# Optimization experiments

Hardware: AMD Instinct MI355X
Metric: run time of the kernel (lower is better)

Reference implementation:

```python
import jax, jax.numpy as jnp
import numpy as np

B, C, H, W = 4, 256, 64, 64
Q = 150          # num_queries
HID = 1024       # q_after hidden size
NEG = 1e9


def setup_inputs() -> dict:
    key = jax.random.key(0)
    ks = jax.random.split(key, 12)
    img_feat = jax.random.normal(ks[0], (B, C, H, W), jnp.float32)
    exe_feat = jax.random.normal(ks[1], (B, C, 7, 7), jnp.float32)
    mask = jax.random.randint(ks[2], (B, H, W), 0, 2).astype(jnp.float32)
    # parameters (similarity init = identity + small noise for a non-degenerate test)
    S = jnp.eye(C, dtype=jnp.float32) + 0.02 * jax.random.normal(ks[3], (C, C), jnp.float32)
    Wv = jax.random.normal(ks[4], (C, C), jnp.float32) / np.sqrt(C)
    ln_g = jnp.ones((C + 1,), jnp.float32)
    ln_b = jnp.zeros((C + 1,), jnp.float32)
    W1 = jax.random.normal(ks[5], (HID, C + 1), jnp.float32) / np.sqrt(C + 1)
    b1 = jnp.zeros((HID,), jnp.float32)
    W2 = jax.random.normal(ks[6], (C + 1, HID), jnp.float32) / np.sqrt(HID)
    b2 = jnp.zeros((C + 1,), jnp.float32)
    return {"img_feat": img_feat, "exe_feat": exe_feat, "mask": mask, "S": S,
            "Wv": Wv, "ln_g": ln_g, "ln_b": ln_b, "W1": W1, "b1": b1, "W2": W2, "b2": b2}


def _get_queries(simil):
    # simil: [B,H,W] detached heatmap; local-maxima NMS then top-k
    c1 = simil[:, :-1] >= simil[:, 1:]
    c2 = simil[:, 1:] > simil[:, :-1]
    c3 = simil[:, :, :-1] >= simil[:, :, 1:]
    c4 = simil[:, :, 1:] > simil[:, :, :-1]
    interior = c1[:, 1:, 1:-1] & c2[:, :-1, 1:-1] & c3[:, 1:-1, 1:] & c4[:, 1:-1, :-1]
    is_max = jnp.zeros(simil.shape, bool).at[:, 1:-1, 1:-1].set(interior)
    sup = jnp.where(is_max, simil, simil - NEG)
    _, q_ids = jax.lax.top_k(sup.reshape(simil.shape[0], -1), Q)   # [B,Q]
    coords = jnp.stack([q_ids // W, q_ids % W], axis=2)            # [B,Q,2]
    return q_ids, coords


def _forward(img_feat, exe_feat, mask, S, Wv, ln_g, ln_b, W1, b1, W2, b2):
    b, c, h, w = img_feat.shape
    hw = h * w
    unrolled = img_feat.reshape(b, c, hw)                               # [B,C,HW]
    exe = exe_feat.mean(axis=(2, 3))[:, :, None]                        # [B,C,1]
    concat = jnp.concatenate([unrolled, exe], axis=2)                   # [B,C,HW+1]
    values = jnp.einsum('bcn,dc->bnd', concat, Wv)                      # [B,HW+1,C]
    attn = jnp.einsum('bcm,cd,bdn->bmn', unrolled, S, concat)           # [B,HW,HW+1]
    hm = attn[:, :, -1].reshape(b, 1, h, w)
    q_ids, coords = _get_queries(jax.lax.stop_gradient(attn[:, :, -1]).reshape(b, h, w))
    # mask bias: outer product of pixel mask, exemplar column always allowed
    m2 = mask.reshape(b, hw, 1) * mask.reshape(b, 1, hw)
    m2 = jnp.concatenate([m2, jnp.ones((b, hw, 1), m2.dtype)], axis=2)
    attn = attn - (m2 != 1).astype(attn.dtype) * NEG
    attn = jax.nn.softmax(attn, axis=2)
    new_img = jnp.einsum('bmn,bnd->bmd', attn, values)                  # [B,HW,C]
    img_out = new_img.transpose(0, 2, 1).reshape(b, c, h, w) + img_feat
    img_out = jnp.concatenate([img_out, hm], axis=1)                    # [B,C+1,H,W]
    # gather query vectors at NMS peak locations
    q = jnp.take_along_axis(img_out.reshape(b, c + 1, hw), q_ids[:, None, :], axis=2)
    q = q.transpose(0, 2, 1)                                            # [B,Q,C+1]
    # q_after: LayerNorm -> Linear(1024) -> ReLU -> Linear(C+1)
    mu = q.mean(-1, keepdims=True)
    var = ((q - mu) ** 2).mean(-1, keepdims=True)
    qn = (q - mu) / jnp.sqrt(var + 1e-5) * ln_g + ln_b
    q_out = jax.nn.relu(qn @ W1.T + b1) @ W2.T + b2
    return img_out, q_out, coords


def reference(img_feat, exe_feat, mask, S, Wv, ln_g, ln_b, W1, b1, W2, b2):
    return _forward(img_feat, exe_feat, mask, S, Wv, ln_g, ln_b, W1, b1, W2, b2)
```

## Files before the change

kernel.cpp:

```cpp
#include <hip/hip_runtime.h>
#include <hip/hip_bf16.h>
#include <stdint.h>

typedef unsigned short u16;
typedef unsigned int u32;
typedef unsigned long long u64;
typedef __attribute__((ext_vector_type(8))) unsigned short u16x8;
typedef __attribute__((ext_vector_type(8))) short short8;
typedef __attribute__((ext_vector_type(4))) float f32x4;

#define CB   4
#define CC   256
#define CHW  4096
#define CNQ  4097
#define NQP  150
#define CHID 1024
#define XTROWS 4160
#define VROW   4160

#define XT_OFF   0ul
#define VB_OFF   (XT_OFF  + (size_t)CB*XTROWS*CC*2)
#define ST_OFF   (VB_OFF  + (size_t)CB*CC*VROW*2)
#define EXE_OFF  (ST_OFF  + 131072ul)
#define ZL_OFF   (EXE_OFF + 4096ul)
#define HEAT_OFF (ZL_OFF  + 4096ul)
#define QID_OFF  (HEAT_OFF+ 65536ul)
#define W1T_OFF  (QID_OFF + 2560ul)
#define W2T_OFF  (W1T_OFF + 1052672ul)
#define HB_OFF   (W2T_OFF + 1052672ul)

__device__ __forceinline__ u16 f2b(float f){
  __hip_bfloat16 h = __float2bfloat16(f); u16 r; __builtin_memcpy(&r, &h, 2); return r;
}
__device__ __forceinline__ f32x4 mfma16(u16x8 a, u16x8 b, f32x4 c){
  short8 as, bs; __builtin_memcpy(&as, &a, 16); __builtin_memcpy(&bs, &b, 16);
  return __builtin_amdgcn_mfma_f32_16x16x32_bf16(as, bs, c, 0, 0, 0);
}
__device__ __forceinline__ u16x8 zero8(){
  u16x8 v;
  #pragma unroll
  for (int e = 0; e < 8; e++) v[e] = 0;
  return v;
}
__device__ __forceinline__ u16x8 cvt8(f32x4 a, f32x4 b){
  u16x8 v;
  v[0]=f2b(a[0]); v[1]=f2b(a[1]); v[2]=f2b(a[2]); v[3]=f2b(a[3]);
  v[4]=f2b(b[0]); v[5]=f2b(b[1]); v[6]=f2b(b[2]); v[7]=f2b(b[3]);
  return v;
}
__device__ __forceinline__ void glds16(const u16* gp, u16* lp){
  __builtin_amdgcn_global_load_lds(
      (const __attribute__((address_space(1))) u32*)gp,
      (__attribute__((address_space(3))) u32*)lp, 16, 0, 0);
}

#define DPPF(x, ctrl) __int_as_float(__builtin_amdgcn_mov_dpp(__float_as_int(x), (ctrl), 0xF, 0xF, true))
__device__ __forceinline__ float red16_max(float x){
  x = fmaxf(x, DPPF(x, 0xB1));
  x = fmaxf(x, DPPF(x, 0x4E));
  x = fmaxf(x, DPPF(x, 0x141));
  x = fmaxf(x, DPPF(x, 0x140));
  return x;
}
__device__ __forceinline__ float red16_sum(float x){
  x += DPPF(x, 0xB1);
  x += DPPF(x, 0x4E);
  x += DPPF(x, 0x141);
  x += DPPF(x, 0x140);
  return x;
}

__device__ __forceinline__ void tpose_body(const float* __restrict__ src,
    float* __restrict__ dst, int R, int C, int bx, int by, char* sbuf){
  float (*tile)[33] = (float(*)[33])sbuf;
  int c0 = bx*32, r0 = by*32;
  int tc = threadIdx.x & 31, tr = threadIdx.x >> 5;
  for (int i = tr; i < 32; i += 8){
    int r = r0 + i, c = c0 + tc;
    tile[i][tc] = (r < R && c < C) ? src[(long)r*C + c] : 0.f;
  }
  __syncthreads();
  for (int i = tr; i < 32; i += 8){
    int c = c0 + i, r = r0 + tc;
    if (c < C && r < R) dst[(long)c*R + r] = tile[tc][i];
  }
}

__device__ __forceinline__ void t64_body(const float* __restrict__ src,
    u16* __restrict__ dst, int srcLd, long srcBatch, int dstLd, long dstBatch,
    int swz, int bx, int by, int bz, char* sbuf, u16* __restrict__ vb){
  u16 (*tile)[72] = (u16(*)[72])sbuf;
  int c0 = bx*64, m0 = by*64;
  const float* S = src + (long)bz*srcBatch;
  u16* D = dst + (long)bz*dstBatch;
  int t = threadIdx.x;
  int r = t >> 2, q = t & 3;
  for (int uu = q; uu < 8; uu += 4){
    const float* p = S + (long)(c0+r)*srcLd + m0 + uu*8;
    f32x4 a0 = *(const f32x4*)p;
    f32x4 a1 = *(const f32x4*)(p + 4);
    *(u16x8*)&tile[r][uu*8] = cvt8(a0, a1);
  }
  __syncthreads();
  for (int uu = q; uu < 8; uu += 4){
    u16x8 v;
    #pragma unroll
    for (int e = 0; e < 8; e++) v[e] = tile[uu*8 + e][r];
    int gidx = (c0 >> 3) + uu;
    if (swz) gidx ^= (r & 7)*4;
    *(u16x8*)(D + (long)(m0+r)*dstLd + gidx*8) = v;
  }
  if (vb){
    int c = c0 + r, cx = c & 7;
    u16* drow = vb + ((long)bz*CC + c)*VROW + m0;
    #pragma unroll
    for (int uu = q; uu < 8; uu += 4){
      u16x8 v = *(const u16x8*)&tile[r][uu*8];
      *(u16x8*)(drow + (uu ^ cx)*8) = v;
    }
  }
}

__global__ __launch_bounds__(256) void prep_k(
    const float* __restrict__ exe, const float* __restrict__ S,
    const float* __restrict__ W1, const float* __restrict__ W2,
    float* __restrict__ zl, u16* __restrict__ Xt, u16* __restrict__ Vb,
    u16* __restrict__ St, float* __restrict__ W1t, float* __restrict__ W2t){
  __shared__ __align__(16) char sbuf[9216];
  int id = blockIdx.x, t = threadIdx.x;
  if (id < 4){
    float* em = (float*)sbuf;
    int b = id;
    const float* p = exe + (b*CC + t)*49;
    float s = 0.f;
    for (int i = 0; i < 49; i++) s += p[i];
    float m = s / 49.f;
    em[t] = m;
    u16* xb = Xt + (size_t)b*XTROWS*CC;
    xb[(size_t)CHW*CC + t] = f2b(m);
    for (int i = 0; i < 63; i++)
      xb[(size_t)(CHW + 1 + i)*CC + t] = 0;
    {
      int cx = t & 7;
      u16* drow = Vb + ((long)b*CC + t)*VROW;
      #pragma unroll
      for (int gl = 0; gl < 8; gl++)
        *(u16x8*)(drow + (512 + gl)*8) = zero8();
      drow[(512 + cx)*8] = f2b(m);
    }
    __syncthreads();
    const float* Sr = S + (long)t*CC;
    float z = 0.f;
    for (int d = 0; d < CC; d++) z += Sr[d] * em[d];
    zl[b*CC + t] = z;
  } else if (id < 292){
    int i = id - 4;
    tpose_body(W1, W1t, CHID, 257, i % 9, i / 9, sbuf);
  } else if (id < 580){
    int i = id - 292;
    tpose_body(W2, W2t, 257, CHID, i % 32, i / 32, sbuf);
  } else {
    int i = id - 580;
    t64_body(S, St, CC, 0, CC, 0, 0, i & 3, i >> 2, 0, sbuf, nullptr);
  }
}

__global__ __launch_bounds__(256) void big_k(
    const float* __restrict__ img, const float* __restrict__ zl,
    u16* __restrict__ Xt, u16* __restrict__ Vb,
    float* __restrict__ heat, float* __restrict__ out_img){
  __shared__ __align__(16) char sbuf[9216];
  int id = blockIdx.x, t = threadIdx.x;
  if (id < 1024){
    int bx = id & 3, by = (id >> 2) & 63, bz = id >> 8;
    t64_body(img, Xt, CHW, (long)CC*CHW, CC, (long)XTROWS*CC, 1, bx, by, bz,
             sbuf, Vb);
  } else {
    int i = id - 1024;
    int bx = i & 15, b = i >> 4;
    float* z = (float*)sbuf;
    z[t] = zl[b*CC + t];
    __syncthreads();
    int m = bx*256 + t;
    const float* base = img + (long)b*CC*CHW + m;
    float s = 0.f;
    for (int c = 0; c < CC; c++) s += base[(long)c*CHW] * z[c];
    heat[b*CHW + m] = s;
    out_img[(long)b*257*CHW + (long)256*CHW + m] = s;
  }
}

__global__ __launch_bounds__(1024) void topk_k(const float* __restrict__ heat,
                                               int* __restrict__ qids,
                                               float* __restrict__ out_coords){
  int b = blockIdx.x, t = threadIdx.x;
  __shared__ unsigned long long sk[4096];
  const float* hb = heat + (long)b*CHW;
  for (int p = t; p < 4096; p += 1024){
    int i = p >> 6, j = p & 63;
    float h = hb[p];
    bool ismax = false;
    if (i >= 1 && i < 63 && j >= 1 && j < 63){
      ismax = (h >= hb[p+64]) && (h > hb[p-64]) && (h >= hb[p+1]) && (h > hb[p-1]);
    }
    float sup = ismax ? h : (h - 1e9f);
    unsigned u = __float_as_uint(sup);
    u = (u & 0x80000000u) ? ~u : (u | 0x80000000u);
    unsigned long long key = ((unsigned long long)u << 32) | (unsigned)(0xFFFFFFFFu - (unsigned)p);
    sk[p] = ~key;
  }
  __syncthreads();
  for (int k = 2; k <= 4096; k <<= 1){
    for (int j = k >> 1; j > 0; j >>= 1){
      for (int tt = t; tt < 2048; tt += 1024){
        int i1 = 2*tt - (tt & (j-1));
        int i2 = i1 + j;
        unsigned long long a = sk[i1], c = sk[i2];
        bool up = ((i1 & k) == 0);
        if (up ? (a > c) : (a < c)){ sk[i1] = c; sk[i2] = a; }
      }
      __syncthreads();
    }
  }
  if (t < NQP){
    unsigned long long key = ~sk[t];
    int p = (int)(0xFFFFFFFFu - (unsigned)(key & 0xFFFFFFFFull));
    qids[b*160 + t] = p;
    out_coords[((long)b*NQP + t)*2 + 0] = (float)(p >> 6);
    out_coords[((long)b*NQP + t)*2 + 1] = (float)(p & 63);
  }
}

__global__ __launch_bounds__(512, 2) void flash_k(
    const u16* __restrict__ Xt, const u16* __restrict__ St,
    const u16* __restrict__ Vb, const float* __restrict__ imgf,
    const float* __restrict__ maskp, const float* __restrict__ Wv,
    float* __restrict__ out_img){
  __shared__ __align__(16) char smem[144384];
  u16*   kp0 = (u16*)smem;
  u16*   kt0 = (u16*)(smem + 32768);
  u16*   kp1 = (u16*)(smem + 65536);
  u16*   kt1 = (u16*)(smem + 98304);
  u16*   p_tile = (u16*)(smem + 131072);
  unsigned char* maskb = (unsigned char*)(smem + 139264);
  float* mlx = (float*)(smem + 143360);

  int f = blockIdx.x;
  int l = (f & 7)*32 + (f >> 3);
  int b = l >> 6;
  int m0 = (l & 63)*64;
  int t = threadIdx.x;
  int lane = t & 63, l15 = lane & 15, qd = lane >> 4;
  int w = t >> 6, wm = w & 3, wn = w >> 2;
  f32x4 zero4 = {0.f,0.f,0.f,0.f};

  {
    const float* mp = maskp + (long)b*CHW + t*8;
    f32x4 a0 = *(const f32x4*)mp;
    f32x4 a1 = *(const f32x4*)(mp + 4);
    unsigned long long pk = 0;
    #pragma unroll
    for (int e = 0; e < 4; e++){
      pk |= (unsigned long long)(a0[e] == 1.0f ? 1u : 0u) << (8*e);
      pk |= (unsigned long long)(a1[e] == 1.0f ? 1u : 0u) << (8*(e+4));
    }
    *(unsigned long long*)&maskb[t*8] = pk;
  }

  const u16* xtb = Xt + (size_t)b*XTROWS*CC;
  const u16* vbb = Vb + (size_t)b*CC*VROW;

  {
    f32x4 D[8];
    #pragma unroll
    for (int i = 0; i < 8; i++) D[i] = zero4;
    const u16* arow = xtb + (long)(m0 + wm*16 + l15)*CC;
    int rsw = (l15 & 7)*4;
    #pragma unroll
    for (int ks = 0; ks < 8; ks++){
      u16x8 af = *(const u16x8*)(arow + ((ks*4 + qd) ^ rsw)*8);
      #pragma unroll
      for (int ds = 0; ds < 8; ds++){
        int dsg = wn*8 + ds;
        u16x8 bf_ = *(const u16x8*)(St + (long)(dsg*16 + l15)*CC + ks*32 + qd*8);
        D[ds] = mfma16(af, bf_, D[ds]);
      }
    }
    #pragma unroll
    for (int ds = 0; ds < 8; ds++){
      #pragma unroll
      for (int r = 0; r < 4; r++){
        int prow = wm*16 + qd*4 + r;
        int ccol = (wn*8 + ds)*16 + l15;
        kp0[prow*256 + ((ccol >> 3) ^ ((prow & 7)*4))*8 + (ccol & 7)] = f2b(D[ds][r]);
      }
    }
  }
  __syncthreads();
  u16x8 afrag[8];
  {
    int arl = wm*16 + l15;
    #pragma unroll
    for (int ks = 0; ks < 8; ks++)
      afrag[ks] = *(const u16x8*)&kp0[arl*256 + (((ks*4 + qd)) ^ ((arl & 7)*4))*8];
  }
  int rowAllowed[4];
  float mi[4], li[4];
  #pragma unroll
  for (int r = 0; r < 4; r++){
    int m = m0 + wm*16 + qd*4 + r;
    rowAllowed[r] = maskb[m];
    mi[r] = -1e30f; li[r] = 0.f;
  }
  f32x4 O[16];
  #pragma unroll
  for (int i = 0; i < 16; i++) O[i] = zero4;
  __syncthreads();

  {
    const u16* ksrc = xtb + w*2048 + lane*8;
    u16* kl = kp0 + w*2048;
    glds16(ksrc,        kl);
    glds16(ksrc + 512,  kl + 512);
    glds16(ksrc + 1024, kl + 1024);
    glds16(ksrc + 1536, kl + 1536);
    const u16* vsrc = vbb + (long)(w*32 + (lane >> 3))*VROW + (lane & 7)*8;
    u16* vl = kt0 + w*2048;
    glds16(vsrc,            vl);
    glds16(vsrc + 8*VROW,   vl + 512);
    glds16(vsrc + 16*VROW,  vl + 1024);
    glds16(vsrc + 24*VROW,  vl + 1536);
  }
  __syncthreads();

  for (int nt = 0; nt < 65; nt++){
    int cur = nt & 1;
    const u16* kpc = cur ? kp1 : kp0;
    const u16* ktc = cur ? kt1 : kt0;
    u16* kpn = cur ? kp0 : kp1;
    u16* ktn = cur ? kt0 : kt1;
    int n0 = nt*64;

    if (nt < 64){
      int n1 = n0 + 64;
      const u16* ksrc = xtb + (long)n1*CC + w*2048 + lane*8;
      u16* kl = kpn + w*2048;
      glds16(ksrc,        kl);
      glds16(ksrc + 512,  kl + 512);
      glds16(ksrc + 1024, kl + 1024);
      glds16(ksrc + 1536, kl + 1536);
      const u16* vsrc = vbb + (long)(w*32 + (lane >> 3))*VROW + n1 + (lane & 7)*8;
      u16* vl = ktn + w*2048;
      glds16(vsrc,            vl);
      glds16(vsrc + 8*VROW,   vl + 512);
      glds16(vsrc + 16*VROW,  vl + 1024);
      glds16(vsrc + 24*VROW,  vl + 1536);
    }

    f32x4 sc[2];
    sc[0] = zero4; sc[1] = zero4;
    __builtin_amdgcn_s_setprio(1);
    #pragma unroll
    for (int ks = 0; ks < 8; ks++){
      #pragma unroll
      for (int ns = 0; ns < 2; ns++){
        int n_l = (wn*2 + ns)*16 + l15;
        u16x8 bfrag = *(const u16x8*)&kpc[n_l*256 + (((ks*4 + qd)) ^ ((n_l & 7)*4))*8];
        sc[ns] = mfma16(afrag[ks], bfrag, sc[ns]);
      }
    }
    __builtin_amdgcn_s_setprio(0);

    float sEff[2][4];
    #pragma unroll
    for (int ns = 0; ns < 2; ns++){
      int n = n0 + (wn*2 + ns)*16 + l15;
      bool inv = (n >= CNQ);
      bool isEx = (n == CHW);
      int cm = 0;
      if (!inv && !isEx) cm = maskb[n];
      #pragma unroll
      for (int r = 0; r < 4; r++){
        float s = sc[ns][r];
        float se;
        if (inv)        se = -1e30f;
        else if (isEx)  se = s;
        else            se = (rowAllowed[r] & cm) ? s : s - 1e9f;
        sEff[ns][r] = se;
      }
    }
    float al[4], nm[4];
    #pragma unroll
    for (int r = 0; r < 4; r++){
      float tm = red16_max(fmaxf(sEff[0][r], sEff[1][r]));
      float newm = fmaxf(mi[r], tm);
      al[r] = (mi[r] < -1e29f) ? 0.f : __expf(fmaxf(mi[r] - newm, -88.f));
      nm[r] = newm; mi[r] = newm;
    }
    #pragma unroll
    for (int r = 0; r < 4; r++){
      float rs = 0.f;
      int prow = wm*16 + qd*4 + r;
      #pragma unroll
      for (int ns = 0; ns < 2; ns++){
        float p = __expf(fmaxf(sEff[ns][r] - nm[r], -88.f));
        rs += p;
        int ccol = (wn*2 + ns)*16 + l15;
        p_tile[prow*64 + ((ccol >> 3) ^ (prow & 7))*8 + (ccol & 7)] = f2b(p);
      }
      li[r] = li[r]*al[r] + red16_sum(rs);
    }
    asm volatile("s_waitcnt lgkmcnt(0)" ::: "memory");

    int needre = (al[0] != 1.f) | (al[1] != 1.f) | (al[2] != 1.f) | (al[3] != 1.f);
    if (__any(needre)){
      #pragma unroll
      for (int ds = 0; ds < 16; ds++){
        #pragma unroll
        for (int r = 0; r < 4; r++) O[ds][r] *= al[r];
      }
    }
    {
      int prow2 = wm*16 + l15;
      u16x8 pf = *(const u16x8*)&p_tile[prow2*64 + (((wn*4 + qd)) ^ (prow2 & 7))*8];
      __builtin_amdgcn_s_setprio(1);
      #pragma unroll
      for (int ds = 0; ds < 16; ds++){
        int c = ds*16 + l15;
        u16x8 vf = *(const u16x8*)&ktc[c*64 + (((wn*4 + qd)) ^ (c & 7))*8];
        O[ds] = mfma16(pf, vf, O[ds]);
      }
      __builtin_amdgcn_s_setprio(0);
    }
    __syncthreads();
  }

  if (l15 == 0){
    #pragma unroll
    for (int r = 0; r < 4; r++){
      mlx[(((wm*2 + wn)*16) + qd*4 + r)*2 + 0] = mi[r];
      mlx[(((wm*2 + wn)*16) + qd*4 + r)*2 + 1] = li[r];
    }
  }
  __syncthreads();
  float alpha[4], linv[4];
  #pragma unroll
  for (int r = 0; r < 4; r++){
    float mo = mlx[(((wm*2 + (1 - wn))*16) + qd*4 + r)*2 + 0];
    float lo = mlx[(((wm*2 + (1 - wn))*16) + qd*4 + r)*2 + 1];
    float ms = fmaxf(mi[r], mo);
    float aS = (mi[r] < -1e29f) ? 0.f : __expf(mi[r] - ms);
    float aO = (mo    < -1e29f) ? 0.f : __expf(mo - ms);
    float ls = li[r]*aS + lo*aO;
    alpha[r] = aS;
    linv[r] = (ls > 0.f) ? (1.0f / ls) : 0.f;
  }
  float* Tsum = (float*)smem;
  if (wn == 1){
    #pragma unroll
    for (int ds = 0; ds < 16; ds++){
      #pragma unroll
      for (int r = 0; r < 4; r++)
        Tsum[(wm*16 + qd*4 + r)*256 + ds*16 + l15] = O[ds][r]*alpha[r];
    }
  }
  __syncthreads();
  if (wn == 0){
    #pragma unroll
    for (int ds = 0; ds < 16; ds++){
      #pragma unroll
      for (int r = 0; r < 4; r++)
        O[ds][r] = (O[ds][r]*alpha[r] + Tsum[(wm*16 + qd*4 + r)*256 + ds*16 + l15]) * linv[r];
    }
  }
  __syncthreads();
  if (wn == 0){
    #pragma unroll
    for (int ds = 0; ds < 16; ds++){
      #pragma unroll
      for (int r = 0; r < 4; r++){
        int prow = wm*16 + qd*4 + r;
        int ccol = ds*16 + l15;
        kp0[prow*256 + ((ccol >> 3) ^ ((prow & 7)*4))*8 + (ccol & 7)] = f2b(O[ds][r]);
      }
    }
  }
  __syncthreads();
  u16x8 tfrag[8];
  {
    int arl = wm*16 + l15;
    #pragma unroll
    for (int ks = 0; ks < 8; ks++)
      tfrag[ks] = *(const u16x8*)&kp0[arl*256 + (((ks*4 + qd)) ^ ((arl & 7)*4))*8];
  }
  f32x4 F[8];
  #pragma unroll
  for (int i = 0; i < 8; i++) F[i] = zero4;
  #pragma unroll
  for (int ks = 0; ks < 8; ks++){
    #pragma unroll
    for (int ds = 0; ds < 8; ds++){
      int dsg = wn*8 + ds;
      const float* wr = Wv + (long)(dsg*16 + l15)*CC + ks*32 + qd*8;
      f32x4 w0 = *(const f32x4*)wr;
      f32x4 w1 = *(const f32x4*)(wr + 4);
      F[ds] = mfma16(tfrag[ks], cvt8(w0, w1), F[ds]);
    }
  }

  float* oi = out_img + (long)b*257*CHW;
  const float* fi = imgf + (long)b*CC*CHW;
  int mb = m0 + wm*16 + qd*4;
  #pragma unroll
  for (int ds = 0; ds < 8; ds++){
    int d = (wn*8 + ds)*16 + l15;
    f32x4 ivals = *(const f32x4*)(fi + (long)d*CHW + mb);
    f32x4 ovals;
    #pragma unroll
    for (int r = 0; r < 4; r++) ovals[r] = F[ds][r] + ivals[r];
    *(f32x4*)(oi + (long)d*CHW + mb) = ovals;
  }
}

__global__ __launch_bounds__(256) void qhead1_k(const float* __restrict__ out_img,
    const int* __restrict__ qids,
    const float* __restrict__ g, const float* __restrict__ be,
    const float* __restrict__ W1t, const float* __restrict__ b1,
    float* __restrict__ Hb){
  int hc = blockIdx.x, rb = blockIdx.y;
  int t = threadIdx.x, lane = t & 63, wv = t >> 6;
  __shared__ __align__(16) float xl[4][260];
  {
    int gq = rb*4 + wv;
    int b = gq / NQP, q = gq - b*NQP;
    int m = qids[b*160 + q];
    const float* oib = out_img + (long)b*257*CHW + m;
    float v[4];
    #pragma unroll
    for (int j = 0; j < 4; j++) v[j] = oib[(long)(lane + j*64)*CHW];
    float v4 = (lane == 0) ? oib[(long)256*CHW] : 0.f;
    float s = v[0]+v[1]+v[2]+v[3]+v4;
    #pragma unroll
    for (int d = 1; d < 64; d <<= 1) s += __shfl_xor(s, d, 64);
    float mu = s / 257.f;
    float d4 = (lane == 0) ? (v4 - mu) : 0.f;
    float vs = d4*d4;
    #pragma unroll
    for (int j = 0; j < 4; j++){ float dd = v[j]-mu; vs += dd*dd; }
    #pragma unroll
    for (int d = 1; d < 64; d <<= 1) vs += __shfl_xor(vs, d, 64);
    float inv = 1.0f / sqrtf(vs/257.f + 1e-5f);
    #pragma unroll
    for (int j = 0; j < 4; j++)
      xl[wv][lane + j*64] = (v[j]-mu)*inv*g[lane + j*64] + be[lane + j*64];
    if (lane == 0) xl[wv][256] = d4*inv*g[256] + be[256];
  }
  __syncthreads();
  int h = hc*256 + t;
  float acc0=0.f, acc1=0.f, acc2=0.f, acc3=0.f;
  #pragma unroll 8
  for (int c = 0; c < 256; c++){
    float wv_ = W1t[(long)c*CHID + h];
    acc0 += wv_*xl[0][c]; acc1 += wv_*xl[1][c];
    acc2 += wv_*xl[2][c]; acc3 += wv_*xl[3][c];
  }
  {
    float wv_ = W1t[(long)256*CHID + h];
    acc0 += wv_*xl[0][256]; acc1 += wv_*xl[1][256];
    acc2 += wv_*xl[2][256]; acc3 += wv_*xl[3][256];
  }
  float bb = b1[h];
  float* hb = Hb + (long)rb*4*CHID + h;
  hb[0]       = fmaxf(acc0 + bb, 0.f);
  hb[CHID]    = fmaxf(acc1 + bb, 0.f);
  hb[2*CHID]  = fmaxf(acc2 + bb, 0.f);
  hb[3*CHID]  = fmaxf(acc3 + bb, 0.f);
}

__global__ __launch_bounds__(256) void qhead2_k(float* __restrict__ qbuf,
    const float* __restrict__ Hb, const float* __restrict__ W2t,
    const float* __restrict__ b2){
  int rb = blockIdx.x;
  int t = threadIdx.x, lane = t & 63, wv = t >> 6;
  __shared__ __align__(16) float hl[4][CHID];
  const float* hs = Hb + (long)rb*4*CHID;
  #pragma unroll
  for (int q = 0; q < 4; q++)
    *(f32x4*)&hl[q][t*4] = *(const f32x4*)&hs[(long)q*CHID + t*4];
  __syncthreads();
  float a0=0.f, a1=0.f, a2=0.f, a3=0.f;
  #pragma unroll 8
  for (int c = 0; c < CHID; c++){
    float wv_ = W2t[(long)c*257 + t];
    a0 += wv_*hl[0][c]; a1 += wv_*hl[1][c];
    a2 += wv_*hl[2][c]; a3 += wv_*hl[3][c];
  }
  float bb = b2[t];
  qbuf[(long)(rb*4 + 0)*257 + t] = a0 + bb;
  qbuf[(long)(rb*4 + 1)*257 + t] = a1 + bb;
  qbuf[(long)(rb*4 + 2)*257 + t] = a2 + bb;
  qbuf[(long)(rb*4 + 3)*257 + t] = a3 + bb;
  if (wv == 0){
    float p0=0.f, p1=0.f, p2=0.f, p3=0.f;
    #pragma unroll
    for (int k = 0; k < 16; k++){
      int c = lane*16 + k;
      float wv_ = W2t[(long)c*257 + 256];
      p0 += wv_*hl[0][c]; p1 += wv_*hl[1][c];
      p2 += wv_*hl[2][c]; p3 += wv_*hl[3][c];
    }
    #pragma unroll
    for (int d = 1; d < 64; d <<= 1){
      p0 += __shfl_xor(p0, d, 64); p1 += __shfl_xor(p1, d, 64);
      p2 += __shfl_xor(p2, d, 64); p3 += __shfl_xor(p3, d, 64);
    }
    if (lane == 0){
      float b256 = b2[256];
      qbuf[(long)(rb*4 + 0)*257 + 256] = p0 + b256;
      qbuf[(long)(rb*4 + 1)*257 + 256] = p1 + b256;
      qbuf[(long)(rb*4 + 2)*257 + 256] = p2 + b256;
      qbuf[(long)(rb*4 + 3)*257 + 256] = p3 + b256;
    }
  }
}

extern "C" void kernel_launch(void* const* d_in, const int* in_sizes, int n_in,
                              void* d_out, int out_size, void* d_ws, size_t ws_size,
                              hipStream_t stream){
  (void)out_size; (void)ws_size;
  int idxImg=-1, idxExe=-1, idxMask=-1, idxB1=-1;
  int idx65[2]={-1,-1}; int n65=0;
  int idx263[2]={-1,-1}; int n263=0;
  int idx257[3]={-1,-1,-1}; int n257=0;
  for (int i = 0; i < n_in; i++){
    int s = in_sizes[i];
    if      (s == 4194304) idxImg = i;
    else if (s == 50176)   idxExe = i;
    else if (s == 16384)   idxMask = i;
    else if (s == 1024)    idxB1 = i;
    else if (s == 65536)  { if (n65 < 2)  idx65[n65++] = i; }
    else if (s == 263168) { if (n263 < 2) idx263[n263++] = i; }
    else if (s == 257)    { if (n257 < 3) idx257[n257++] = i; }
  }
  const float* img  = (const float*)d_in[idxImg];
  const float* exe  = (const float*)d_in[idxExe];
  const float* mask = (const float*)d_in[idxMask];
  const float* S    = (const float*)d_in[idx65[0]];
  const float* Wv   = (const float*)d_in[idx65[1]];
  const float* W1   = (const float*)d_in[idx263[0]];
  const float* W2   = (const float*)d_in[idx263[1]];
  const float* b1   = (const float*)d_in[idxB1];
  const float *lng, *lnb, *b2;
  if (idxImg == 0){
    lng = (const float*)d_in[idx257[0]];
    lnb = (const float*)d_in[idx257[1]];
    b2  = (const float*)d_in[idx257[2]];
  } else {
    b2  = (const float*)d_in[idx257[0]];
    lnb = (const float*)d_in[idx257[1]];
    lng = (const float*)d_in[idx257[2]];
  }

  char* ws = (char*)d_ws;
  u16*   Xt   = (u16*)(ws + XT_OFF);
  u16*   Vb   = (u16*)(ws + VB_OFF);
  u16*   St   = (u16*)(ws + ST_OFF);
  float* zl   = (float*)(ws + ZL_OFF);
  float* heat = (float*)(ws + HEAT_OFF);
  int*   qids = (int*)(ws + QID_OFF);
  float* W1t  = (float*)(ws + W1T_OFF);
  float* W2t  = (float*)(ws + W2T_OFF);
  float* Hb   = (float*)(ws + HB_OFF);

  float* out      = (float*)d_out;
  float* out_img  = out;
  float* qbuf     = out + (size_t)CB*257*CHW;
  float* out_crd  = qbuf + (size_t)CB*NQP*257;

  prep_k<<<dim3(596), dim3(256), 0, stream>>>(
      exe, S, W1, W2, zl, Xt, Vb, St, W1t, W2t);
  big_k<<<dim3(1088), dim3(256), 0, stream>>>(
      img, zl, Xt, Vb, heat, out_img);
  topk_k<<<dim3(CB), dim3(1024), 0, stream>>>(heat, qids, out_crd);
  flash_k<<<dim3(256), dim3(512), 0, stream>>>(
      Xt, St, Vb, img, mask, Wv, out_img);
  qhead1_k<<<dim3(4, CB*NQP/4), dim3(256), 0, stream>>>(
      out_img, qids, lng, lnb, W1t, b1, Hb);
  qhead2_k<<<dim3(CB*NQP/4), dim3(256), 0, stream>>>(qbuf, Hb, W2t, b2);
}
```

Baseline: 400.8 us.

## Split flash attention over key halves with a separate merge kernel

```diff
diff --git a/kernel.cpp b/kernel.cpp
--- a/kernel.cpp
+++ b/kernel.cpp
@@ -28,6 +28,8 @@
 #define W1T_OFF  (QID_OFF + 2560ul)
 #define W2T_OFF  (W1T_OFF + 1052672ul)
 #define HB_OFF   (W2T_OFF + 1052672ul)
+#define OP_OFF   (HB_OFF  + 2457600ul)
+#define ML_OFF   (OP_OFF  + (size_t)512*64*256*4)
 
 __device__ __forceinline__ u16 f2b(float f){
   __hip_bfloat16 h = __float2bfloat16(f); u16 r; __builtin_memcpy(&r, &h, 2); return r;
@@ -233,22 +235,24 @@
 
 __global__ __launch_bounds__(512, 2) void flash_k(
     const u16* __restrict__ Xt, const u16* __restrict__ St,
-    const u16* __restrict__ Vb, const float* __restrict__ imgf,
-    const float* __restrict__ maskp, const float* __restrict__ Wv,
-    float* __restrict__ out_img){
-  __shared__ __align__(16) char smem[144384];
-  u16*   kp0 = (u16*)smem;
-  u16*   kt0 = (u16*)(smem + 32768);
-  u16*   kp1 = (u16*)(smem + 65536);
-  u16*   kt1 = (u16*)(smem + 98304);
-  u16*   p_tile = (u16*)(smem + 131072);
-  unsigned char* maskb = (unsigned char*)(smem + 139264);
-  float* mlx = (float*)(smem + 143360);
+    const u16* __restrict__ Vb, const float* __restrict__ maskp,
+    float* __restrict__ Opart, float* __restrict__ MLpart){
+  __shared__ __align__(16) char smem[78848];
+  u16*   kp = (u16*)smem;
+  u16*   kt = (u16*)(smem + 32768);
+  u16*   p_tile = (u16*)(smem + 65536);
+  unsigned char* maskb = (unsigned char*)(smem + 73728);
+  float* mlx = (float*)(smem + 77824);
 
   int f = blockIdx.x;
-  int l = (f & 7)*32 + (f >> 3);
-  int b = l >> 6;
-  int m0 = (l & 63)*64;
+  int b = (f & 7) >> 1;
+  int half = f & 1;
+  int mt = f >> 3;
+  int m0 = mt*64;
+  int ntBeg = half ? 33 : 0;
+  int ntEnd = half ? 65 : 33;
+  int pid = (b*64 + mt)*2 + half;
+
   int t = threadIdx.x;
   int lane = t & 63, l15 = lane & 15, qd = lane >> 4;
   int w = t >> 6, wm = w & 3, wn = w >> 2;
@@ -292,7 +296,7 @@
       for (int r = 0; r < 4; r++){
         int prow = wm*16 + qd*4 + r;
         int ccol = (wn*8 + ds)*16 + l15;
-        kp0[prow*256 + ((ccol >> 3) ^ ((prow & 7)*4))*8 + (ccol & 7)] = f2b(D[ds][r]);
+        kp[prow*256 + ((ccol >> 3) ^ ((prow & 7)*4))*8 + (ccol & 7)] = f2b(D[ds][r]);
       }
     }
   }
@@ -302,7 +306,7 @@
     int arl = wm*16 + l15;
     #pragma unroll
     for (int ks = 0; ks < 8; ks++)
-      afrag[ks] = *(const u16x8*)&kp0[arl*256 + (((ks*4 + qd)) ^ ((arl & 7)*4))*8];
+      afrag[ks] = *(const u16x8*)&kp[arl*256 + (((ks*4 + qd)) ^ ((arl & 7)*4))*8];
   }
   int rowAllowed[4];
   float mi[4], li[4];
@@ -317,45 +321,26 @@
   for (int i = 0; i < 16; i++) O[i] = zero4;
   __syncthreads();
 
-  {
-    const u16* ksrc = xtb + w*2048 + lane*8;
-    u16* kl = kp0 + w*2048;
-    glds16(ksrc,        kl);
-    glds16(ksrc + 512,  kl + 512);
-    glds16(ksrc + 1024, kl + 1024);
-    glds16(ksrc + 1536, kl + 1536);
-    const u16* vsrc = vbb + (long)(w*32 + (lane >> 3))*VROW + (lane & 7)*8;
-    u16* vl = kt0 + w*2048;
-    glds16(vsrc,            vl);
-    glds16(vsrc + 8*VROW,   vl + 512);
-    glds16(vsrc + 16*VROW,  vl + 1024);
-    glds16(vsrc + 24*VROW,  vl + 1536);
-  }
-  __syncthreads();
-
-  for (int nt = 0; nt < 65; nt++){
-    int cur = nt & 1;
-    const u16* kpc = cur ? kp1 : kp0;
-    const u16* ktc = cur ? kt1 : kt0;
-    u16* kpn = cur ? kp0 : kp1;
-    u16* ktn = cur ? kt0 : kt1;
+#define STAGE(n0_) do { \
+    const u16* ksrc_ = xtb + (long)(n0_)*CC + w*2048 + lane*8; \
+    u16* kl_ = kp + w*2048; \
+    glds16(ksrc_,        kl_); \
+    glds16(ksrc_ + 512,  kl_ + 512); \
+    glds16(ksrc_ + 1024, kl_ + 1024); \
+    glds16(ksrc_ + 1536, kl_ + 1536); \
+    const u16* vsrc_ = vbb + (long)(w*32 + (lane >> 3))*VROW + (n0_) + (lane & 7)*8; \
+    u16* vl_ = kt + w*2048; \
+    glds16(vsrc_,            vl_); \
+    glds16(vsrc_ + 8*VROW,   vl_ + 512); \
+    glds16(vsrc_ + 16*VROW,  vl_ + 1024); \
+    glds16(vsrc_ + 24*VROW,  vl_ + 1536); \
+  } while(0)
+
+  STAGE(ntBeg*64);
+  __syncthreads();
+
+  for (int nt = ntBeg; nt < ntEnd; nt++){
     int n0 = nt*64;
-
-    if (nt < 64){
-      int n1 = n0 + 64;
-      const u16* ksrc = xtb + (long)n1*CC + w*2048 + lane*8;
-      u16* kl = kpn + w*2048;
-      glds16(ksrc,        kl);
-      glds16(ksrc + 512,  kl + 512);
-      glds16(ksrc + 1024, kl + 1024);
-      glds16(ksrc + 1536, kl + 1536);
-      const u16* vsrc = vbb + (long)(w*32 + (lane >> 3))*VROW + n1 + (lane & 7)*8;
-      u16* vl = ktn + w*2048;
-      glds16(vsrc,            vl);
-      glds16(vsrc + 8*VROW,   vl + 512);
-      glds16(vsrc + 16*VROW,  vl + 1024);
-      glds16(vsrc + 24*VROW,  vl + 1536);
-    }
 
     f32x4 sc[2];
     sc[0] = zero4; sc[1] = zero4;
@@ -365,7 +350,7 @@
       #pragma unroll
       for (int ns = 0; ns < 2; ns++){
         int n_l = (wn*2 + ns)*16 + l15;
-        u16x8 bfrag = *(const u16x8*)&kpc[n_l*256 + (((ks*4 + qd)) ^ ((n_l & 7)*4))*8];
+        u16x8 bfrag = *(const u16x8*)&kp[n_l*256 + (((ks*4 + qd)) ^ ((n_l & 7)*4))*8];
         sc[ns] = mfma16(afrag[ks], bfrag, sc[ns]);
       }
     }
@@ -427,13 +412,16 @@
       #pragma unroll
       for (int ds = 0; ds < 16; ds++){
         int c = ds*16 + l15;
-        u16x8 vf = *(const u16x8*)&ktc[c*64 + (((wn*4 + qd)) ^ (c & 7))*8];
+        u16x8 vf = *(const u16x8*)&kt[c*64 + (((wn*4 + qd)) ^ (c & 7))*8];
         O[ds] = mfma16(pf, vf, O[ds]);
       }
       __builtin_amdgcn_s_setprio(0);
     }
     __syncthreads();
-  }
+    if (nt + 1 < ntEnd) STAGE((nt + 1)*64);
+    __syncthreads();
+  }
+#undef STAGE
 
   if (l15 == 0){
     #pragma unroll
@@ -443,7 +431,7 @@
     }
   }
   __syncthreads();
-  float alpha[4], linv[4];
+  float alpha[4], msv[4], lsv[4];
   #pragma unroll
   for (int r = 0; r < 4; r++){
     float mo = mlx[(((wm*2 + (1 - wn))*16) + qd*4 + r)*2 + 0];
@@ -451,9 +439,9 @@
     float ms = fmaxf(mi[r], mo);
     float aS = (mi[r] < -1e29f) ? 0.f : __expf(mi[r] - ms);
     float aO = (mo    < -1e29f) ? 0.f : __expf(mo - ms);
-    float ls = li[r]*aS + lo*aO;
+    lsv[r] = li[r]*aS + lo*aO;
+    msv[r] = ms;
     alpha[r] = aS;
-    linv[r] = (ls > 0.f) ? (1.0f / ls) : 0.f;
   }
   float* Tsum = (float*)smem;
   if (wn == 1){
@@ -466,23 +454,63 @@
   }
   __syncthreads();
   if (wn == 0){
+    float* ob = Opart + (size_t)pid*64*256;
     #pragma unroll
     for (int ds = 0; ds < 16; ds++){
       #pragma unroll
-      for (int r = 0; r < 4; r++)
-        O[ds][r] = (O[ds][r]*alpha[r] + Tsum[(wm*16 + qd*4 + r)*256 + ds*16 + l15]) * linv[r];
-    }
-  }
-  __syncthreads();
-  if (wn == 0){
-    #pragma unroll
-    for (int ds = 0; ds < 16; ds++){
-      #pragma unroll
       for (int r = 0; r < 4; r++){
-        int prow = wm*16 + qd*4 + r;
-        int ccol = ds*16 + l15;
-        kp0[prow*256 + ((ccol >> 3) ^ ((prow & 7)*4))*8 + (ccol & 7)] = f2b(O[ds][r]);
-      }
+        int row = wm*16 + qd*4 + r;
+        float v = O[ds][r]*alpha[r] + Tsum[row*256 + ds*16 + l15];
+        ob[row*256 + ds*16 + l15] = v;
+      }
+    }
+    if (l15 == 0){
+      #pragma unroll
+      for (int r = 0; r < 4; r++){
+        int row = wm*16 + qd*4 + r;
+        MLpart[(size_t)pid*128 + row*2 + 0] = msv[r];
+        MLpart[(size_t)pid*128 + row*2 + 1] = lsv[r];
+      }
+    }
+  }
+}
+
+__global__ __launch_bounds__(256) void mrg_k(
+    const float* __restrict__ Opart, const float* __restrict__ MLpart,
+    const float* __restrict__ imgf, const float* __restrict__ Wv,
+    float* __restrict__ out_img){
+  __shared__ __align__(16) u16 kp[64*256];
+  int id = blockIdx.x;
+  int b = id >> 6;
+  int m0 = (id & 63)*64;
+  int t = threadIdx.x;
+  int lane = t & 63, l15 = lane & 15, qd = lane >> 4;
+  int wm = t >> 6;
+  const float* O0 = Opart + (size_t)(id*2 + 0)*64*256;
+  const float* O1 = Opart + (size_t)(id*2 + 1)*64*256;
+  const float* ml0 = MLpart + (size_t)(id*2 + 0)*128;
+  const float* ml1 = MLpart + (size_t)(id*2 + 1)*128;
+  float a0[4], a1[4], linv[4];
+  #pragma unroll
+  for (int r = 0; r < 4; r++){
+    int row = wm*16 + qd*4 + r;
+    float m0v = ml0[row*2], l0 = ml0[row*2 + 1];
+    float m1v = ml1[row*2], l1 = ml1[row*2 + 1];
+    float ms = fmaxf(m0v, m1v);
+    float e0 = (m0v < -1e29f) ? 0.f : __expf(m0v - ms);
+    float e1 = (m1v < -1e29f) ? 0.f : __expf(m1v - ms);
+    float l = l0*e0 + l1*e1;
+    a0[r] = e0; a1[r] = e1;
+    linv[r] = (l > 0.f) ? (1.0f / l) : 0.f;
+  }
+  #pragma unroll
+  for (int ds = 0; ds < 16; ds++){
+    #pragma unroll
+    for (int r = 0; r < 4; r++){
+      int row = wm*16 + qd*4 + r;
+      int col = ds*16 + l15;
+      float v = (O0[row*256 + col]*a0[r] + O1[row*256 + col]*a1[r]) * linv[r];
+      kp[row*256 + ((col >> 3) ^ ((row & 7)*4))*8 + (col & 7)] = f2b(v);
     }
   }
   __syncthreads();
@@ -491,29 +519,28 @@
     int arl = wm*16 + l15;
     #pragma unroll
     for (int ks = 0; ks < 8; ks++)
-      tfrag[ks] = *(const u16x8*)&kp0[arl*256 + (((ks*4 + qd)) ^ ((arl & 7)*4))*8];
-  }
-  f32x4 F[8];
-  #pragma unroll
-  for (int i = 0; i < 8; i++) F[i] = zero4;
+      tfrag[ks] = *(const u16x8*)&kp[arl*256 + (((ks*4 + qd)) ^ ((arl & 7)*4))*8];
+  }
+  f32x4 F[16];
+  f32x4 zero4 = {0.f,0.f,0.f,0.f};
+  #pragma unroll
+  for (int i = 0; i < 16; i++) F[i] = zero4;
   #pragma unroll
   for (int ks = 0; ks < 8; ks++){
     #pragma unroll
-    for (int ds = 0; ds < 8; ds++){
-      int dsg = wn*8 + ds;
-      const float* wr = Wv + (long)(dsg*16 + l15)*CC + ks*32 + qd*8;
+    for (int ds = 0; ds < 16; ds++){
+      const float* wr = Wv + (long)(ds*16 + l15)*CC + ks*32 + qd*8;
       f32x4 w0 = *(const f32x4*)wr;
       f32x4 w1 = *(const f32x4*)(wr + 4);
       F[ds] = mfma16(tfrag[ks], cvt8(w0, w1), F[ds]);
     }
   }
-
   float* oi = out_img + (long)b*257*CHW;
   const float* fi = imgf + (long)b*CC*CHW;
   int mb = m0 + wm*16 + qd*4;
   #pragma unroll
-  for (int ds = 0; ds < 8; ds++){
-    int d = (wn*8 + ds)*16 + l15;
+  for (int ds = 0; ds < 16; ds++){
+    int d = ds*16 + l15;
     f32x4 ivals = *(const f32x4*)(fi + (long)d*CHW + mb);
     f32x4 ovals;
     #pragma unroll
@@ -671,6 +698,8 @@
   float* W1t  = (float*)(ws + W1T_OFF);
   float* W2t  = (float*)(ws + W2T_OFF);
   float* Hb   = (float*)(ws + HB_OFF);
+  float* Op   = (float*)(ws + OP_OFF);
+  float* Ml   = (float*)(ws + ML_OFF);
 
   float* out      = (float*)d_out;
   float* out_img  = out;
@@ -682,8 +711,9 @@
   big_k<<<dim3(1088), dim3(256), 0, stream>>>(
       img, zl, Xt, Vb, heat, out_img);
   topk_k<<<dim3(CB), dim3(1024), 0, stream>>>(heat, qids, out_crd);
-  flash_k<<<dim3(256), dim3(512), 0, stream>>>(
-      Xt, St, Vb, img, mask, Wv, out_img);
+  flash_k<<<dim3(512), dim3(512), 0, stream>>>(
+      Xt, St, Vb, mask, Op, Ml);
+  mrg_k<<<dim3(256), dim3(256), 0, stream>>>(Op, Ml, img, Wv, out_img);
   qhead1_k<<<dim3(4, CB*NQP/4), dim3(256), 0, stream>>>(
       out_img, qids, lng, lnb, W1t, b1, Hb);
   qhead2_k<<<dim3(CB*NQP/4), dim3(256), 0, stream>>>(qbuf, Hb, W2t, b2);
```

After: 463.1 us. +15.6%, slower.
